# Kernel tuning notes

Hardware: AMD Instinct MI355X
Metric: run time of the kernel (lower is better)

Reference implementation:

```python
import jax, jax.numpy as jnp
import numpy as np

D = 768
H = 12
HD = D // H
HID = 3072
EPS = 1e-5


def layer_norm(x, g, b):
    m = jnp.mean(x, axis=-1, keepdims=True)
    v = jnp.mean((x - m) ** 2, axis=-1, keepdims=True)
    return (x - m) * jax.lax.rsqrt(v + EPS) * g + b


def setup_inputs() -> dict:
    key = jax.random.key(0)
    ks = jax.random.split(key, 8)
    s_in = 1.0 / np.sqrt(D)
    s_hid = 1.0 / np.sqrt(HID)
    return {
        "x": jax.random.normal(ks[0], (32, 577, D), dtype=jnp.float32),
        "w_qkv": jax.random.normal(ks[1], (D, 3 * D), dtype=jnp.float32) * s_in,
        "b_qkv": jnp.zeros((3 * D,), dtype=jnp.float32),
        "w_proj": jax.random.normal(ks[2], (D, D), dtype=jnp.float32) * s_in,
        "b_proj": jnp.zeros((D,), dtype=jnp.float32),
        "g1": jnp.ones((D,), jnp.float32), "be1": jnp.zeros((D,), jnp.float32),
        "g2": jnp.ones((D,), jnp.float32), "be2": jnp.zeros((D,), jnp.float32),
        "g3": jnp.ones((D,), jnp.float32), "be3": jnp.zeros((D,), jnp.float32),
        "w1": jax.random.normal(ks[3], (D, HID), dtype=jnp.float32) * s_in,
        "bm1": jnp.zeros((HID,), dtype=jnp.float32),
        "w2": jax.random.normal(ks[4], (HID, D), dtype=jnp.float32) * s_hid,
        "bm2": jnp.zeros((D,), dtype=jnp.float32),
    }


def reference(x, w_qkv, b_qkv, w_proj, b_proj, g1, be1, g2, be2, g3, be3, w1, bm1, w2, bm2):
    B, N, _ = x.shape
    scale = 1.0 / np.sqrt(HD).astype(np.float32)

    # --- attention block ---
    h = layer_norm(x, g1, be1)
    qkv = h @ w_qkv + b_qkv                       # [B,N,3D]
    q, k, v = jnp.split(qkv, 3, axis=-1)
    q = q.reshape(B, N, H, HD).transpose(0, 2, 1, 3)  # [B,H,N,hd]
    k = k.reshape(B, N, H, HD).transpose(0, 2, 1, 3)
    v = v.reshape(B, N, H, HD).transpose(0, 2, 1, 3)
    scores = jnp.einsum("bhnd,bhmd->bhnm", q, k) * scale  # materialized O(N^2), as in source
    probs = jax.nn.softmax(scores, axis=-1)
    attn = jnp.einsum("bhnm,bhmd->bhnd", probs, v)
    attn = attn.transpose(0, 2, 1, 3).reshape(B, N, D)
    attn = attn @ w_proj + b_proj
    res1 = x + attn

    # --- MLP block (note: source applies LayerNorm2 AND the MLP's own LayerNorm) ---
    h = layer_norm(res1, g2, be2)
    h = layer_norm(h, g3, be3)
    h = jax.nn.gelu(h @ w1 + bm1, approximate=False)
    h = h @ w2 + bm2  # dropout = identity at eval
    return res1 + h
```

## Files before the change

kernel.cpp:

```cpp
#include <hip/hip_runtime.h>
#include <hip/hip_bf16.h>


#define M_ROWS 18464
#define NHEAD 12

typedef __attribute__((ext_vector_type(8))) short s16x8;
typedef __attribute__((ext_vector_type(4))) float f32x4;

__device__ __forceinline__ unsigned short f2bf(float f) {
  union { float f; unsigned u; } v; v.f = f;
  return (unsigned short)((v.u + 0x7fffu + ((v.u >> 16) & 1u)) >> 16);
}
__device__ __forceinline__ float bf2f(unsigned short h) {
  union { unsigned u; float f; } v; v.u = ((unsigned)h) << 16;
  return v.f;
}

__device__ __forceinline__ void gload_lds16(const void* g, void* l) {
  __builtin_amdgcn_global_load_lds((const __attribute__((address_space(1))) unsigned*)g,
                                   (__attribute__((address_space(3))) unsigned*)l, 16, 0, 0);
}

__global__ __launch_bounds__(256) void wtrans(const float* __restrict__ in,
                                              unsigned short* __restrict__ out,
                                              int K, int N) {
  __shared__ float t[32][33];
  const int n0 = blockIdx.x * 32, k0 = blockIdx.y * 32;
  const int tx = threadIdx.x, ty = threadIdx.y;
  for (int i = ty; i < 32; i += 8)
    t[i][tx] = in[(size_t)(k0 + i) * N + n0 + tx];
  __syncthreads();
  for (int i = ty; i < 32; i += 8)
    out[(size_t)(n0 + i) * K + k0 + tx] = f2bf(t[tx][i]);
}

__global__ __launch_bounds__(256) void ln1_kernel(const float* __restrict__ x,
    const float* __restrict__ g, const float* __restrict__ be,
    unsigned short* __restrict__ out) {
  const int w = threadIdx.x >> 6, l = threadIdx.x & 63;
  const size_t row = (size_t)blockIdx.x * 4 + w;
  const float* xr = x + row * 768;
  f32x4 v[3];
#pragma unroll
  for (int s = 0; s < 3; s++) v[s] = ((const f32x4*)xr)[s * 64 + l];
  float sm = 0.f, sq = 0.f;
#pragma unroll
  for (int s = 0; s < 3; s++)
#pragma unroll
    for (int j = 0; j < 4; j++) { sm += v[s][j]; sq += v[s][j] * v[s][j]; }
#pragma unroll
  for (int o = 1; o < 64; o <<= 1) { sm += __shfl_xor(sm, o); sq += __shfl_xor(sq, o); }
  const float mean = sm * (1.f / 768.f);
  const float rs = rsqrtf(sq * (1.f / 768.f) - mean * mean + 1e-5f);
  unsigned short* orow = out + row * 768;
#pragma unroll
  for (int s = 0; s < 3; s++) {
    int col = s * 256 + l * 4;
    unsigned short h4[4];
#pragma unroll
    for (int j = 0; j < 4; j++)
      h4[j] = f2bf((v[s][j] - mean) * rs * g[col + j] + be[col + j]);
    uint2 u; u.x = h4[0] | ((unsigned)h4[1] << 16); u.y = h4[2] | ((unsigned)h4[3] << 16);
    *(uint2*)(orow + col) = u;
  }
}

__global__ __launch_bounds__(256) void ln2_kernel(const float* __restrict__ xin,
    const float* __restrict__ g2, const float* __restrict__ be2,
    const float* __restrict__ g3, const float* __restrict__ be3,
    unsigned short* __restrict__ out) {
  const int w = threadIdx.x >> 6, l = threadIdx.x & 63;
  const size_t row = (size_t)blockIdx.x * 4 + w;
  const float* xr = xin + row * 768;
  f32x4 v[3];
#pragma unroll
  for (int s = 0; s < 3; s++) v[s] = ((const f32x4*)xr)[s * 64 + l];
  float sm = 0.f, sq = 0.f;
#pragma unroll
  for (int s = 0; s < 3; s++)
#pragma unroll
    for (int j = 0; j < 4; j++) { sm += v[s][j]; sq += v[s][j] * v[s][j]; }
#pragma unroll
  for (int o = 1; o < 64; o <<= 1) { sm += __shfl_xor(sm, o); sq += __shfl_xor(sq, o); }
  float mean = sm * (1.f / 768.f);
  float rs = rsqrtf(sq * (1.f / 768.f) - mean * mean + 1e-5f);
  float y[12];
  sm = 0.f; sq = 0.f;
#pragma unroll
  for (int s = 0; s < 3; s++) {
    int col = s * 256 + l * 4;
#pragma unroll
    for (int j = 0; j < 4; j++) {
      float t = (v[s][j] - mean) * rs * g2[col + j] + be2[col + j];
      y[s * 4 + j] = t; sm += t; sq += t * t;
    }
  }
#pragma unroll
  for (int o = 1; o < 64; o <<= 1) { sm += __shfl_xor(sm, o); sq += __shfl_xor(sq, o); }
  mean = sm * (1.f / 768.f);
  rs = rsqrtf(sq * (1.f / 768.f) - mean * mean + 1e-5f);
  unsigned short* orow = out + row * 768;
#pragma unroll
  for (int s = 0; s < 3; s++) {
    int col = s * 256 + l * 4;
    unsigned short h4[4];
#pragma unroll
    for (int j = 0; j < 4; j++)
      h4[j] = f2bf((y[s * 4 + j] - mean) * rs * g3[col + j] + be3[col + j]);
    uint2 u; u.x = h4[0] | ((unsigned)h4[1] << 16); u.y = h4[2] | ((unsigned)h4[3] << 16);
    *(uint2*)(orow + col) = u;
  }
}

template<int EPI>
__global__ __launch_bounds__(256) void gemm_nt(
    const unsigned short* __restrict__ A, const unsigned short* __restrict__ BT,
    const float* __restrict__ bias, const float* __restrict__ aux,
    void* __restrict__ Cout, int M, int N, int K) {
  __shared__ unsigned short As[2][128 * 32];
  __shared__ unsigned short Bs[2][128 * 32];
  const int tid = threadIdx.x;
  const int w = tid >> 6, l = tid & 63;
  const int gx = (int)gridDim.x;
  const int nwg = gx * (int)gridDim.y;
  const int orig = (int)blockIdx.y * gx + (int)blockIdx.x;
  const int q = nwg >> 3, r = nwg & 7, xcd = orig & 7, slot = orig >> 3;
  const int newid = (xcd < r ? xcd * (q + 1) : r * (q + 1) + (xcd - r) * q) + slot;
  const int m0 = (newid / gx) * 128, n0 = (newid % gx) * 128;

  const int r0 = w * 32 + (l >> 2);
  const int kof = (l & 3) * 8;
  const int lr = l & 15, lg = l >> 4;
  const int wr = (w >> 1) * 64, wc = (w & 1) * 64;
  const int woff = w * 2048;
  f32x4 acc[4][4];
#pragma unroll
  for (int m = 0; m < 4; m++)
#pragma unroll
    for (int n = 0; n < 4; n++)
#pragma unroll
      for (int r4 = 0; r4 < 4; r4++) acc[m][n][r4] = 0.f;

  int ar0 = m0 + r0;      if (ar0 >= M) ar0 = M - 1;
  int ar1 = m0 + r0 + 16; if (ar1 >= M) ar1 = M - 1;
  const size_t a0 = (size_t)ar0 * K + kof;
  const size_t a1 = (size_t)ar1 * K + kof;
  const size_t b0 = (size_t)(n0 + r0) * K + kof;
  const size_t b1 = (size_t)(n0 + r0 + 16) * K + kof;

  gload_lds16(A + a0, (char*)As[0] + woff);
  gload_lds16(A + a1, (char*)As[0] + woff + 1024);
  gload_lds16(BT + b0, (char*)Bs[0] + woff);
  gload_lds16(BT + b1, (char*)Bs[0] + woff + 1024);
  __syncthreads();

  int cur = 0;
  for (int k0 = 0; k0 < K; k0 += 32) {
    const int kn = k0 + 32;
    if (kn < K) {
      gload_lds16(A + a0 + kn, (char*)As[cur ^ 1] + woff);
      gload_lds16(A + a1 + kn, (char*)As[cur ^ 1] + woff + 1024);
      gload_lds16(BT + b0 + kn, (char*)Bs[cur ^ 1] + woff);
      gload_lds16(BT + b1 + kn, (char*)Bs[cur ^ 1] + woff + 1024);
    }
    const char* AsB = (const char*)As[cur];
    const char* BsB = (const char*)Bs[cur];
    s16x8 af[4], bf[4];
#pragma unroll
    for (int m = 0; m < 4; m++)
      af[m] = *(const s16x8*)(AsB + (wr + m * 16 + lr) * 64 + lg * 16);
#pragma unroll
    for (int n = 0; n < 4; n++)
      bf[n] = *(const s16x8*)(BsB + (wc + n * 16 + lr) * 64 + lg * 16);
#pragma unroll
    for (int m = 0; m < 4; m++)
#pragma unroll
      for (int n = 0; n < 4; n++)
        acc[m][n] = __builtin_amdgcn_mfma_f32_16x16x32_bf16(af[m], bf[n], acc[m][n], 0, 0, 0);
    __syncthreads();
    cur ^= 1;
  }

  float bs[4];
#pragma unroll
  for (int n = 0; n < 4; n++) bs[n] = bias[n0 + wc + n * 16 + lr];
#pragma unroll
  for (int m = 0; m < 4; m++) {
#pragma unroll
    for (int r4 = 0; r4 < 4; r4++) {
      int row = m0 + wr + m * 16 + lg * 4 + r4;
      if (row >= M) continue;
      size_t rb = (size_t)row * N;
#pragma unroll
      for (int n = 0; n < 4; n++) {
        int col = n0 + wc + n * 16 + lr;
        float c = acc[m][n][r4] + bs[n];
        if (EPI == 0) {
          ((unsigned short*)Cout)[rb + col] = f2bf(c);
        } else if (EPI == 1) {
          ((float*)Cout)[rb + col] = c + aux[rb + col];
        } else if (EPI == 2) {
          c = 0.5f * c * (1.f + erff(c * 0.70710678118f));
          ((unsigned short*)Cout)[rb + col] = f2bf(c);
        } else {
          ((float*)Cout)[rb + col] = c + aux[rb + col];
        }
      }
    }
  }
}

__global__ __launch_bounds__(256) void attn_kernel(const unsigned short* __restrict__ qkv,
                                                   unsigned short* __restrict__ out) {
  __shared__ unsigned short Pl[4 * 16 * 72];
  __shared__ unsigned short VT[64 * 72];
  const int tid = threadIdx.x;
  const int w = tid >> 6, l = tid & 63;
  const int lr = l & 15, lg = l >> 4;
  const int bh = blockIdx.x / 10, qt = blockIdx.x % 10;
  const int b = bh / NHEAD, h = bh % NHEAD;
  const size_t base = (size_t)b * 577 * 2304 + (size_t)h * 64;
  int qr = qt * 64 + w * 16 + lr; int qrc = qr > 576 ? 576 : qr;
  const unsigned short* qp = qkv + base + (size_t)qrc * 2304;
  const s16x8 qf0 = *(const s16x8*)(qp + lg * 8);
  const s16x8 qf1 = *(const s16x8*)(qp + 32 + lg * 8);
  f32x4 oacc[4];
#pragma unroll
  for (int d = 0; d < 4; d++)
#pragma unroll
    for (int r = 0; r < 4; r++) oacc[d][r] = 0.f;
  float mrun = -3e38f, lrun = 0.f;
  unsigned short* Pw = Pl + w * 16 * 72;

  for (int kt = 0; kt < 10; kt++) {
    __syncthreads();
#pragma unroll
    for (int c = 0; c < 2; c++) {
      int cid = c * 256 + tid;
      int kc = cid >> 3, d0 = (cid & 7) * 8;
      int vr = kt * 64 + kc; if (vr > 576) vr = 576;
      s16x8 vv = *(const s16x8*)(qkv + base + 1536 + (size_t)vr * 2304 + d0);
#pragma unroll
      for (int j = 0; j < 8; j++)
        VT[(d0 + j) * 72 + kc] = (unsigned short)vv[j];
    }
    float sv[16];
#pragma unroll
    for (int sub = 0; sub < 4; sub++) {
      int kc = kt * 64 + sub * 16 + lr; if (kc > 576) kc = 576;
      const unsigned short* kp = qkv + base + 768 + (size_t)kc * 2304;
      s16x8 kf0 = *(const s16x8*)(kp + lg * 8);
      s16x8 kf1 = *(const s16x8*)(kp + 32 + lg * 8);
      f32x4 st;
#pragma unroll
      for (int r = 0; r < 4; r++) st[r] = 0.f;
      st = __builtin_amdgcn_mfma_f32_16x16x32_bf16(kf0, qf0, st, 0, 0, 0);
      st = __builtin_amdgcn_mfma_f32_16x16x32_bf16(kf1, qf1, st, 0, 0, 0);
#pragma unroll
      for (int r = 0; r < 4; r++) {
        int kcg = kt * 64 + sub * 16 + lg * 4 + r;
        sv[sub * 4 + r] = (kcg <= 576) ? st[r] * 0.125f : -3e38f;
      }
    }
    float tm = sv[0];
#pragma unroll
    for (int i = 1; i < 16; i++) tm = fmaxf(tm, sv[i]);
    tm = fmaxf(tm, __shfl_xor(tm, 16));
    tm = fmaxf(tm, __shfl_xor(tm, 32));
    float mnew = fmaxf(mrun, tm);
    float fac = __expf(mrun - mnew);
    mrun = mnew;
    float ts = 0.f;
    unsigned short pb[16];
#pragma unroll
    for (int i = 0; i < 16; i++) {
      float p = __expf(sv[i] - mnew);
      ts += p;
      pb[i] = f2bf(p);
    }
    ts += __shfl_xor(ts, 16);
    ts += __shfl_xor(ts, 32);
    lrun = lrun * fac + ts;
#pragma unroll
    for (int sub = 0; sub < 4; sub++) {
      uint2 u;
      u.x = (unsigned)pb[sub * 4 + 0] | ((unsigned)pb[sub * 4 + 1] << 16);
      u.y = (unsigned)pb[sub * 4 + 2] | ((unsigned)pb[sub * 4 + 3] << 16);
      *(uint2*)(Pw + lr * 72 + sub * 16 + lg * 4) = u;
    }
    float fr[4];
#pragma unroll
    for (int r = 0; r < 4; r++) fr[r] = __shfl(fac, lg * 4 + r);
#pragma unroll
    for (int d = 0; d < 4; d++)
#pragma unroll
      for (int r = 0; r < 4; r++) oacc[d][r] *= fr[r];
    __syncthreads();
#pragma unroll
    for (int hf = 0; hf < 2; hf++) {
      s16x8 pf = *(const s16x8*)(Pw + lr * 72 + hf * 32 + lg * 8);
#pragma unroll
      for (int d = 0; d < 4; d++) {
        s16x8 vf = *(const s16x8*)(VT + (d * 16 + lr) * 72 + hf * 32 + lg * 8);
        oacc[d] = __builtin_amdgcn_mfma_f32_16x16x32_bf16(pf, vf, oacc[d], 0, 0, 0);
      }
    }
  }
#pragma unroll
  for (int r = 0; r < 4; r++) {
    int qg = qt * 64 + w * 16 + lg * 4 + r;
    if (qg > 576) continue;
    float inv = 1.f / __shfl(lrun, lg * 4 + r);
#pragma unroll
    for (int d = 0; d < 4; d++)
      out[(size_t)(b * 577 + qg) * 768 + h * 64 + d * 16 + lr] = f2bf(oacc[d][r] * inv);
  }
}

extern "C" void kernel_launch(void* const* d_in, const int* in_sizes, int n_in,
                              void* d_out, int out_size, void* d_ws, size_t ws_size,
                              hipStream_t stream) {
  const float* x      = (const float*)d_in[0];
  const float* w_qkv  = (const float*)d_in[1];
  const float* b_qkv  = (const float*)d_in[2];
  const float* w_proj = (const float*)d_in[3];
  const float* b_proj = (const float*)d_in[4];
  const float* g1  = (const float*)d_in[5];
  const float* be1 = (const float*)d_in[6];
  const float* g2  = (const float*)d_in[7];
  const float* be2 = (const float*)d_in[8];
  const float* g3  = (const float*)d_in[9];
  const float* be3 = (const float*)d_in[10];
  const float* w1  = (const float*)d_in[11];
  const float* bm1 = (const float*)d_in[12];
  const float* w2  = (const float*)d_in[13];
  const float* bm2 = (const float*)d_in[14];

  char* ws = (char*)d_ws;
  unsigned short* wqkvT  = (unsigned short*)(ws + 0);
  unsigned short* wprojT = (unsigned short*)(ws + 3538944);
  unsigned short* w1T    = (unsigned short*)(ws + 4718592);
  unsigned short* w2T    = (unsigned short*)(ws + 9437184);
  unsigned short* hbuf   = (unsigned short*)(ws + 14155776);
  unsigned short* qkv    = (unsigned short*)(ws + 42516480);
  unsigned short* hid    = qkv;
  unsigned short* attnb  = hbuf;
  float*          res1   = (float*)(ws + 155959296);

  dim3 b32(32, 8);
  wtrans<<<dim3(2304 / 32, 768 / 32),  b32, 0, stream>>>(w_qkv,  wqkvT,  768, 2304);
  wtrans<<<dim3(768 / 32, 768 / 32),   b32, 0, stream>>>(w_proj, wprojT, 768, 768);
  wtrans<<<dim3(3072 / 32, 768 / 32),  b32, 0, stream>>>(w1,     w1T,    768, 3072);
  wtrans<<<dim3(768 / 32, 3072 / 32),  b32, 0, stream>>>(w2,     w2T,    3072, 768);

  ln1_kernel<<<4616, 256, 0, stream>>>(x, g1, be1, hbuf);
  gemm_nt<0><<<dim3(18, 145), 256, 0, stream>>>(hbuf, wqkvT, b_qkv, nullptr, qkv, M_ROWS, 2304, 768);
  attn_kernel<<<3840, 256, 0, stream>>>(qkv, attnb);
  gemm_nt<1><<<dim3(6, 145), 256, 0, stream>>>(attnb, wprojT, b_proj, x, res1, M_ROWS, 768, 768);
  ln2_kernel<<<4616, 256, 0, stream>>>(res1, g2, be2, g3, be3, hbuf);
  gemm_nt<2><<<dim3(24, 145), 256, 0, stream>>>(hbuf, w1T, bm1, nullptr, hid, M_ROWS, 3072, 768);
  gemm_nt<3><<<dim3(6, 145), 256, 0, stream>>>(hid, w2T, bm2, res1, (float*)d_out, M_ROWS, 768, 3072);
}
```

Baseline: 819.9 us.

## Triple-buffer GEMM LDS tiles with explicit vmcnt waits for deeper prefetch

Replaces the double-buffered GEMM main loop with a three-stage LDS ring. Two tiles are now in flight while one is computed, and hand-placed s_waitcnt vmcnt counts plus raw s_barrier calls replace __syncthreads. The aim is to hide more global-load latency behind the MFMA work. In exchange, LDS use per block rises by half, which may lower occupancy, and correctness now depends on the compiler not reordering the manual waitcnt and barrier sequence.

```diff
diff --git a/kernel.cpp b/kernel.cpp
--- a/kernel.cpp
+++ b/kernel.cpp
@@ -118,8 +118,8 @@
     const unsigned short* __restrict__ A, const unsigned short* __restrict__ BT,
     const float* __restrict__ bias, const float* __restrict__ aux,
     void* __restrict__ Cout, int M, int N, int K) {
-  __shared__ unsigned short As[2][128 * 32];
-  __shared__ unsigned short Bs[2][128 * 32];
+  __shared__ unsigned short As[3][128 * 32];
+  __shared__ unsigned short Bs[3][128 * 32];
   const int tid = threadIdx.x;
   const int w = tid >> 6, l = tid & 63;
   const int gx = (int)gridDim.x;
@@ -149,23 +149,27 @@
   const size_t b0 = (size_t)(n0 + r0) * K + kof;
   const size_t b1 = (size_t)(n0 + r0 + 16) * K + kof;
 
-  gload_lds16(A + a0, (char*)As[0] + woff);
-  gload_lds16(A + a1, (char*)As[0] + woff + 1024);
-  gload_lds16(BT + b0, (char*)Bs[0] + woff);
-  gload_lds16(BT + b1, (char*)Bs[0] + woff + 1024);
-  __syncthreads();
-
-  int cur = 0;
-  for (int k0 = 0; k0 < K; k0 += 32) {
-    const int kn = k0 + 32;
-    if (kn < K) {
-      gload_lds16(A + a0 + kn, (char*)As[cur ^ 1] + woff);
-      gload_lds16(A + a1 + kn, (char*)As[cur ^ 1] + woff + 1024);
-      gload_lds16(BT + b0 + kn, (char*)Bs[cur ^ 1] + woff);
-      gload_lds16(BT + b1 + kn, (char*)Bs[cur ^ 1] + woff + 1024);
-    }
-    const char* AsB = (const char*)As[cur];
-    const char* BsB = (const char*)Bs[cur];
+  const int nt = K >> 5;
+#pragma unroll
+  for (int t = 0; t < 3; t++) {
+    const int kk = t << 5;
+    char* ab = (char*)As + t * 8192 + woff;
+    char* bb = (char*)Bs + t * 8192 + woff;
+    gload_lds16(A + a0 + kk, ab);
+    gload_lds16(A + a1 + kk, ab + 1024);
+    gload_lds16(BT + b0 + kk, bb);
+    gload_lds16(BT + b1 + kk, bb + 1024);
+  }
+
+  for (int t = 0; t < nt; t++) {
+    if (t < nt - 2)       asm volatile("s_waitcnt vmcnt(8)" ::: "memory");
+    else if (t == nt - 2) asm volatile("s_waitcnt vmcnt(4)" ::: "memory");
+    else                  asm volatile("s_waitcnt vmcnt(0)" ::: "memory");
+    __builtin_amdgcn_s_barrier();
+
+    const int buf = t - (t / 3) * 3;
+    const char* AsB = (const char*)As + buf * 8192;
+    const char* BsB = (const char*)Bs + buf * 8192;
     s16x8 af[4], bf[4];
 #pragma unroll
     for (int m = 0; m < 4; m++)
@@ -178,8 +182,18 @@
 #pragma unroll
       for (int n = 0; n < 4; n++)
         acc[m][n] = __builtin_amdgcn_mfma_f32_16x16x32_bf16(af[m], bf[n], acc[m][n], 0, 0, 0);
-    __syncthreads();
-    cur ^= 1;
+
+    asm volatile("" ::: "memory");
+    __builtin_amdgcn_s_barrier();
+    if (t + 3 < nt) {
+      const int kk = (t + 3) << 5;
+      char* ab = (char*)As + buf * 8192 + woff;
+      char* bb = (char*)Bs + buf * 8192 + woff;
+      gload_lds16(A + a0 + kk, ab);
+      gload_lds16(A + a1 + kk, ab + 1024);
+      gload_lds16(BT + b0 + kk, bb);
+      gload_lds16(BT + b1 + kk, bb + 1024);
+    }
   }
 
   float bs[4];
```

Result: no change. 807.5 us (-1.5%).
